# Performance work log

Measured on AMD Instinct MI355X. Metric: run time of the kernel, lower is better.

Reference implementation:

```python
import jax, jax.numpy as jnp
import numpy as np

N = 20000      # nodes
E = 160000     # edges (before self loops)
IN = 128       # in_channels (== edge_dim)
H = 8          # heads
C = 64         # out_channels per head
NEG_SLOPE = 0.2


def setup_inputs() -> dict:
    key = jax.random.key(0)
    ks = jax.random.split(key, 8)
    s_in = np.float32(1.0 / np.sqrt(IN))
    s_att = np.float32(1.0 / np.sqrt(C))
    return {
        "x": jax.random.normal(ks[0], (N, IN), jnp.float32),
        "edge_index": jax.random.randint(ks[1], (2, E), 0, N, dtype=jnp.int32),
        "edge_attr": jax.random.normal(ks[2], (E, IN), jnp.float32),
        "Wl": jax.random.normal(ks[3], (IN, H * C), jnp.float32) * s_in,
        "Wr": jax.random.normal(ks[4], (IN, H * C), jnp.float32) * s_in,
        "We": jax.random.normal(ks[5], (IN, H * C), jnp.float32) * s_in,
        "att": jax.random.normal(ks[6], (H, C), jnp.float32) * s_att,
        "bias": jnp.zeros((H * C,), jnp.float32),
    }


def reference(x, edge_index, edge_attr, Wl, Wr, We, att, bias):
    n = x.shape[0]
    e = edge_attr.shape[0]
    src, dst = edge_index[0], edge_index[1]

    # add self loops; self-loop edge_attr = per-target-node mean of incoming
    # edge attrs (PyG fill_value='mean'); nodes with no in-edges get zeros.
    cnt = jax.ops.segment_sum(jnp.ones((e,), x.dtype), dst, num_segments=n)
    loop_attr = jax.ops.segment_sum(edge_attr, dst, num_segments=n) / jnp.maximum(cnt, 1.0)[:, None]
    loops = jnp.arange(n, dtype=src.dtype)
    src_f = jnp.concatenate([src, loops])          # [E+N]
    dst_f = jnp.concatenate([dst, loops])          # [E+N]
    ea = jnp.concatenate([edge_attr, loop_attr], axis=0)  # [E+N, IN]

    xl = (x @ Wl).reshape(n, H, C)   # source projection
    xr = (x @ Wr).reshape(n, H, C)   # target projection
    xe = (ea @ We).reshape(-1, H, C)  # edge projection

    # GATv2 score: att . LeakyReLU(xl_j + xr_i + xe)
    m = jax.nn.leaky_relu(xl[src_f] + xr[dst_f] + xe, NEG_SLOPE)  # [E+N, H, C]
    logits = jnp.einsum('ehc,hc->eh', m, att)                      # [E+N, H]

    # segment softmax over incoming edges of each target node
    lmax = jax.ops.segment_max(logits, dst_f, num_segments=n)      # [N, H]
    p = jnp.exp(logits - lmax[dst_f])
    denom = jax.ops.segment_sum(p, dst_f, num_segments=n)
    alpha = p / denom[dst_f]                                       # [E+N, H]

    # weighted scatter-add aggregation of source features
    out = jax.ops.segment_sum(alpha[:, :, None] * xl[src_f], dst_f, num_segments=n)
    return out.reshape(n, H * C) + bias
```

## Files before the change

### kernel.cpp

```cpp
#include <hip/hip_runtime.h>

#define N_NODES 20000
#define E_EDGES 160000
#define IN_CH 128
#define H_HEADS 8
#define C_CH 64
#define HC 512
#define M_TOT (E_EDGES + N_NODES)
#define NEG_SLOPE 0.2f
#define NCHUNK ((N_NODES + 255) / 256)

typedef __attribute__((ext_vector_type(8))) short bf16x8;
typedef __attribute__((ext_vector_type(4))) float f32x4;

__device__ __forceinline__ unsigned short f2bf(float f) {
    unsigned u = __float_as_uint(f);
    unsigned r = (u + 0x7FFFu + ((u >> 16) & 1u)) >> 16;
    return (unsigned short)r;
}
__device__ __forceinline__ float bf2f(unsigned short s) {
    return __uint_as_float((unsigned)s << 16);
}
__device__ __forceinline__ float bfx(const bf16x8& v0, const bf16x8& v1, int idx) {
    return bf2f((unsigned short)((idx < 8) ? v0[idx] : v1[idx - 8]));
}

#define GLOAD_LDS16(gsrc, ldst) \
    __builtin_amdgcn_global_load_lds((const __attribute__((address_space(1))) void*)(gsrc), \
                                     (__attribute__((address_space(3))) void*)(ldst), 16, 0, 0)

__global__ void k_deg(const int* __restrict__ ei, int* __restrict__ deg) {
    int e = blockIdx.x * blockDim.x + threadIdx.x;
    if (e >= E_EDGES) return;
    atomicAdd(&deg[ei[E_EDGES + e]], 1);
}

__global__ void k_scan1(const int* __restrict__ deg, int* __restrict__ bsum) {
    __shared__ int red[256];
    int tid = threadIdx.x;
    int i = blockIdx.x * 256 + tid;
    red[tid] = (i < N_NODES) ? deg[i] + 1 : 0;
    __syncthreads();
    for (int off = 128; off > 0; off >>= 1) {
        if (tid < off) red[tid] += red[tid + off];
        __syncthreads();
    }
    if (tid == 0) bsum[blockIdx.x] = red[0];
}

__global__ void k_scan2(const int* __restrict__ bsum, int* __restrict__ boff) {
    if (threadIdx.x == 0) {
        int run = 0;
        for (int b = 0; b < NCHUNK; ++b) { boff[b] = run; run += bsum[b]; }
    }
}

__global__ void k_scan3(const int* __restrict__ deg, const int* __restrict__ boff,
                        int* __restrict__ rowptr, int* __restrict__ cursor,
                        int* __restrict__ eidx, int* __restrict__ src_s,
                        int* __restrict__ dst_s) {
    __shared__ int buf[256];
    int tid = threadIdx.x;
    int i = blockIdx.x * 256 + tid;
    int v = (i < N_NODES) ? deg[i] + 1 : 0;
    buf[tid] = v;
    __syncthreads();
    for (int off = 1; off < 256; off <<= 1) {
        int tv = (tid >= off) ? buf[tid - off] : 0;
        __syncthreads();
        buf[tid] += tv;
        __syncthreads();
    }
    if (i < N_NODES) {
        int excl = boff[blockIdx.x] + buf[tid] - v;
        rowptr[i] = excl;
        eidx[excl] = E_EDGES + i;
        src_s[excl] = i;
        dst_s[excl] = i;
        cursor[i] = excl + 1;
        if (i == N_NODES - 1) rowptr[N_NODES] = excl + v;
    }
}

__global__ void k_fill(const int* __restrict__ ei, int* __restrict__ cursor,
                       int* __restrict__ eidx, int* __restrict__ src_s,
                       int* __restrict__ dst_s) {
    int e = blockIdx.x * blockDim.x + threadIdx.x;
    if (e >= E_EDGES) return;
    int d = ei[E_EDGES + e];
    int slot = atomicAdd(&cursor[d], 1);
    eidx[slot] = e;
    src_s[slot] = ei[e];
    dst_s[slot] = d;
}

__global__ void k_prep(const int* __restrict__ rowptr, const int* __restrict__ eidx,
                       const float* __restrict__ ea, unsigned short* __restrict__ eab) {
    int node = (blockIdx.x * blockDim.x + threadIdx.x) >> 6;
    int lane = threadIdx.x & 63;
    if (node >= N_NODES) return;
    int beg = rowptr[node], end = rowptr[node + 1];
    int cnt = end - beg - 1;
    float s0 = 0.f, s1 = 0.f;
    if (beg + 1 < end) {
        const float* p_nxt = ea + (size_t)eidx[beg + 1] * 128 + lane;
        for (int p = beg + 1; p < end; ++p) {
            const float* cur = p_nxt;
            if (p + 1 < end) p_nxt = ea + (size_t)eidx[p + 1] * 128 + lane;
            float v0 = cur[0], v1 = cur[64];
            s0 += v0; s1 += v1;
            eab[(size_t)p * 128 + lane] = f2bf(v0);
            eab[(size_t)p * 128 + 64 + lane] = f2bf(v1);
        }
    }
    float inv = 1.f / fmaxf((float)cnt, 1.f);
    eab[(size_t)beg * 128 + lane] = f2bf(s0 * inv);
    eab[(size_t)beg * 128 + 64 + lane] = f2bf(s1 * inv);
}

__global__ void k_trans3(const float* __restrict__ Wl, const float* __restrict__ Wr,
                         const float* __restrict__ We,
                         unsigned short* __restrict__ WlT, unsigned short* __restrict__ WrT,
                         unsigned short* __restrict__ WeT) {
    int idx = blockIdx.x * blockDim.x + threadIdx.x;
    if (idx >= HC * IN_CH) return;
    int m = blockIdx.y;
    const float* W = (m == 0) ? Wl : (m == 1) ? Wr : We;
    unsigned short* WT = (m == 0) ? WlT : (m == 1) ? WrT : WeT;
    int n = idx >> 7, k = idx & 127;
    WT[idx] = f2bf(W[(size_t)k * HC + n]);
}

__global__ void k_gemm2(const float* __restrict__ A,
                        const unsigned short* __restrict__ WlT,
                        const unsigned short* __restrict__ WrT,
                        unsigned short* __restrict__ xlb, unsigned short* __restrict__ xrb,
                        int M) {
    __shared__ short As[64 * 128];
    int row0 = blockIdx.x * 64;
    int sel = blockIdx.y >> 1;
    const unsigned short* BT = sel ? WrT : WlT;
    unsigned short* Cb = sel ? xrb : xlb;
    int t = threadIdx.x;
    {
        int row = t >> 2, c0 = (t & 3) * 32;
        int gr = row0 + row;
        int sw = (row & 7) << 4;
        const float* src = A + (size_t)gr * 128 + c0;
        #pragma unroll
        for (int i = 0; i < 4; ++i) {
            bf16x8 v;
            if (gr < M) {
                const float4* p = (const float4*)(src + i * 8);
                float4 f0 = p[0], f1 = p[1];
                v[0] = f2bf(f0.x); v[1] = f2bf(f0.y); v[2] = f2bf(f0.z); v[3] = f2bf(f0.w);
                v[4] = f2bf(f1.x); v[5] = f2bf(f1.y); v[6] = f2bf(f1.z); v[7] = f2bf(f1.w);
            } else {
                #pragma unroll
                for (int j = 0; j < 8; ++j) v[j] = 0;
            }
            int off = row * 256 + (((c0 + i * 8) * 2) ^ sw);
            *(bf16x8*)((char*)As + off) = v;
        }
    }
    __syncthreads();

    int w = t >> 6, l = t & 63;
    int lr = l & 15, lk = l >> 4;
    int col0 = (blockIdx.y & 1) * 256 + w * 64;

    f32x4 acc[4][4];
    #pragma unroll
    for (int mi = 0; mi < 4; ++mi)
        #pragma unroll
        for (int fj = 0; fj < 4; ++fj)
            #pragma unroll
            for (int q = 0; q < 4; ++q) acc[mi][fj][q] = 0.f;

    #pragma unroll
    for (int k0 = 0; k0 < 4; ++k0) {
        bf16x8 a4[4];
        #pragma unroll
        for (int mi = 0; mi < 4; ++mi) {
            int row = mi * 16 + lr;
            int off = row * 256 + ((k0 * 64 + lk * 16) ^ ((row & 7) << 4));
            a4[mi] = *(const bf16x8*)((const char*)As + off);
        }
        #pragma unroll
        for (int fj = 0; fj < 4; ++fj) {
            bf16x8 b = *(const bf16x8*)(BT + (size_t)(col0 + fj * 16 + lr) * 128 + k0 * 32 + lk * 8);
            #pragma unroll
            for (int mi = 0; mi < 4; ++mi)
                acc[mi][fj] = __builtin_amdgcn_mfma_f32_16x16x32_bf16(a4[mi], b, acc[mi][fj], 0, 0, 0);
        }
    }
    #pragma unroll
    for (int mi = 0; mi < 4; ++mi) {
        #pragma unroll
        for (int reg = 0; reg < 4; ++reg) {
            int r = row0 + mi * 16 + lk * 4 + reg;
            if (r < M) {
                unsigned short* cp = Cb + (size_t)r * 512 + col0 + lr;
                #pragma unroll
                for (int fj = 0; fj < 4; ++fj) cp[fj * 16] = f2bf(acc[mi][fj][reg]);
            }
        }
    }
}

#define PREF(R, CB, SLOT) { \
    int s_ = s_src[R], d_ = s_dst[R]; \
    const bf16x8* xp_ = (const bf16x8*)(xlb + (size_t)s_ * 512 + (CB) + q * 16); \
    pa0[SLOT] = xp_[0]; pa1[SLOT] = xp_[1]; \
    const bf16x8* rp_ = (const bf16x8*)(xrb + (size_t)d_ * 512 + (CB) + q * 16); \
    pb0[SLOT] = rp_[0]; pb1[SLOT] = rp_[1]; }

__global__ void k_fused(const int* __restrict__ src_s, const int* __restrict__ dst_s,
                        const int* __restrict__ rowptr,
                        const unsigned short* __restrict__ eab,
                        const unsigned short* __restrict__ WeT,
                        const unsigned short* __restrict__ xlb,
                        const unsigned short* __restrict__ xrb,
                        const float* __restrict__ att, const float* __restrict__ bias,
                        float* __restrict__ logits, float* __restrict__ out) {
    __shared__ short As[64 * 128];
    __shared__ float xeT[4][16][68];
    __shared__ float att_s[512];
    __shared__ float lg[64][8];
    __shared__ int s_src[64], s_dst[64];
    __shared__ int own_node[64], own_beg[64], own_len[64];
    __shared__ int n_own;
    int row0 = blockIdx.x * 64;
    int t = threadIdx.x;

    if (t == 0) n_own = 0;
    __syncthreads();

    {
        int l = t & 63;
        int c_base = (t >> 6) * 4;
        #pragma unroll
        for (int i = 0; i < 4; ++i) {
            int c = c_base + i;
            int row_local = c * 4 + (l >> 4);
            int grow = row0 + row_local;
            if (grow > M_TOT - 1) grow = M_TOT - 1;
            int chunk = (l & 15) ^ (row_local & 7);
            const char* src = (const char*)eab + (size_t)grow * 256 + chunk * 16;
            char* dst = (char*)As + c * 1024;
            GLOAD_LDS16(src, dst);
        }
    }

    if (t < 64) {
        int p = row0 + t;
        int s = 0, d = 0;
        if (p < M_TOT) {
            s = src_s[p]; d = dst_s[p];
            int pb = rowptr[d], pe = rowptr[d + 1];
            if (pb == p && pe <= row0 + 64) {
                int idx = atomicAdd(&n_own, 1);
                own_node[idx] = d; own_beg[idx] = t; own_len[idx] = pe - pb;
            }
        }
        s_src[t] = s; s_dst[t] = d;
    }
    att_s[t] = att[t];
    att_s[t + 256] = att[t + 256];

    asm volatile("s_waitcnt vmcnt(0)");
    __syncthreads();

    int w = t >> 6, l = t & 63;
    int lr = l & 15, lk = l >> 4;
    int eloc = l >> 2, q = l & 3;
    int cb0 = w * 128;

    bf16x8 pa0[2], pa1[2], pb0[2], pb1[2];
    f32x4 acc[4][4];

    PREF(eloc, cb0, 0);

    #pragma unroll
    for (int hh = 0; hh < 2; ++hh) {
        int cb = cb0 + hh * 64;
        int h = w * 2 + hh;

        #pragma unroll
        for (int mi = 0; mi < 4; ++mi)
            #pragma unroll
            for (int fj = 0; fj < 4; ++fj)
                #pragma unroll
                for (int qq = 0; qq < 4; ++qq) acc[mi][fj][qq] = 0.f;

        #pragma unroll
        for (int k0 = 0; k0 < 4; ++k0) {
            bf16x8 a4[4];
            #pragma unroll
            for (int mi = 0; mi < 4; ++mi) {
                int row = mi * 16 + lr;
                int off = row * 256 + ((k0 * 64 + lk * 16) ^ ((row & 7) << 4));
                a4[mi] = *(const bf16x8*)((const char*)As + off);
            }
            #pragma unroll
            for (int fj = 0; fj < 4; ++fj) {
                bf16x8 b = *(const bf16x8*)(WeT + (size_t)(cb + fj * 16 + lr) * 128 + k0 * 32 + lk * 8);
                #pragma unroll
                for (int mi = 0; mi < 4; ++mi)
                    acc[mi][fj] = __builtin_amdgcn_mfma_f32_16x16x32_bf16(a4[mi], b, acc[mi][fj], 0, 0, 0);
            }
        }

        #pragma unroll
        for (int mi = 0; mi < 4; ++mi) {
            if (mi < 3) { PREF(mi * 16 + 16 + eloc, cb, (mi + 1) & 1); }
            else if (hh == 0) { PREF(eloc, cb + 64, 0); }

            #pragma unroll
            for (int fj = 0; fj < 4; ++fj)
                #pragma unroll
                for (int reg = 0; reg < 4; ++reg)
                    xeT[w][lk * 4 + reg][fj * 16 + lr] = acc[mi][fj][reg];

            const bf16x8 ca0 = pa0[mi & 1], ca1 = pa1[mi & 1];
            const bf16x8 cb0v = pb0[mi & 1], cb1v = pb1[mi & 1];

            float sum = 0.f;
            #pragma unroll
            for (int sg = 0; sg < 4; ++sg) {
                float4 xe4 = *(const float4*)&xeT[w][eloc][q * 16 + sg * 4];
                float4 av  = *(const float4*)&att_s[cb + q * 16 + sg * 4];
                float v0 = xe4.x + bfx(ca0, ca1, sg * 4 + 0) + bfx(cb0v, cb1v, sg * 4 + 0);
                float v1 = xe4.y + bfx(ca0, ca1, sg * 4 + 1) + bfx(cb0v, cb1v, sg * 4 + 1);
                float v2 = xe4.z + bfx(ca0, ca1, sg * 4 + 2) + bfx(cb0v, cb1v, sg * 4 + 2);
                float v3 = xe4.w + bfx(ca0, ca1, sg * 4 + 3) + bfx(cb0v, cb1v, sg * 4 + 3);
                v0 = (v0 > 0.f) ? v0 : v0 * NEG_SLOPE;
                v1 = (v1 > 0.f) ? v1 : v1 * NEG_SLOPE;
                v2 = (v2 > 0.f) ? v2 : v2 * NEG_SLOPE;
                v3 = (v3 > 0.f) ? v3 : v3 * NEG_SLOPE;
                sum = fmaf(av.x, v0, sum);
                sum = fmaf(av.y, v1, sum);
                sum = fmaf(av.z, v2, sum);
                sum = fmaf(av.w, v3, sum);
            }
            sum += __shfl_xor(sum, 1, 64);
            sum += __shfl_xor(sum, 2, 64);
            if (q == 0) {
                int rloc = mi * 16 + eloc;
                lg[rloc][h] = sum;
                int p = row0 + rloc;
                if (p < M_TOT) logits[(size_t)p * 8 + h] = sum;
            }
        }
    }
    __syncthreads();

    {
        int lane = t & 63;
        int h = lane >> 3;
        for (int o = w; o < n_own; o += 4) {
            int d = own_node[o], rb = own_beg[o], len = own_len[o];
            float m = -3.4e38f;
            for (int j = 0; j < len; ++j) m = fmaxf(m, lg[rb + j][h]);
            float den = 0.f;
            for (int j = 0; j < len; ++j) den += __expf(lg[rb + j][h] - m);
            float rden = 1.f / den;
            float ac[8] = {};
            bf16x8 v_nxt = *(const bf16x8*)(xlb + (size_t)s_src[rb] * 512 + lane * 8);
            for (int j = 0; j < len; ++j) {
                bf16x8 v = v_nxt;
                if (j + 1 < len)
                    v_nxt = *(const bf16x8*)(xlb + (size_t)s_src[rb + j + 1] * 512 + lane * 8);
                float alpha = __expf(lg[rb + j][h] - m) * rden;
                #pragma unroll
                for (int jj = 0; jj < 8; ++jj) ac[jj] = fmaf(alpha, bf2f((unsigned short)v[jj]), ac[jj]);
            }
            float4* op = (float4*)(out + (size_t)d * 512 + lane * 8);
            const float4* bp = (const float4*)(bias + lane * 8);
            float4 bv0 = bp[0], bv1 = bp[1];
            float4 r0 = { ac[0] + bv0.x, ac[1] + bv0.y, ac[2] + bv0.z, ac[3] + bv0.w };
            float4 r1 = { ac[4] + bv1.x, ac[5] + bv1.y, ac[6] + bv1.z, ac[7] + bv1.w };
            op[0] = r0; op[1] = r1;
        }
    }
}

__global__ void k_cleanup(const int* __restrict__ rowptr, const int* __restrict__ src_s,
                          const float* __restrict__ logits,
                          const unsigned short* __restrict__ xlb, const float* __restrict__ bias,
                          float* __restrict__ out) {
    int node = (blockIdx.x * blockDim.x + threadIdx.x) >> 6;
    int lane = threadIdx.x & 63;
    if (node >= N_NODES) return;
    int beg = rowptr[node], end = rowptr[node + 1];
    if ((beg >> 6) == ((end - 1) >> 6)) return;
    int h = lane >> 3;

    float m = -3.4e38f;
    for (int p = beg; p < end; ++p) m = fmaxf(m, logits[(size_t)p * 8 + h]);
    float den = 0.f;
    for (int p = beg; p < end; ++p) den += __expf(logits[(size_t)p * 8 + h] - m);
    float rden = 1.f / den;

    float acc[8] = {};
    bf16x8 v_nxt = *(const bf16x8*)(xlb + (size_t)src_s[beg] * 512 + lane * 8);
    for (int p = beg; p < end; ++p) {
        bf16x8 v = v_nxt;
        float lgv = logits[(size_t)p * 8 + h];
        if (p + 1 < end)
            v_nxt = *(const bf16x8*)(xlb + (size_t)src_s[p + 1] * 512 + lane * 8);
        float alpha = __expf(lgv - m) * rden;
        #pragma unroll
        for (int j = 0; j < 8; ++j) acc[j] = fmaf(alpha, bf2f((unsigned short)v[j]), acc[j]);
    }
    float4* op = (float4*)(out + (size_t)node * 512 + lane * 8);
    const float4* bp = (const float4*)(bias + lane * 8);
    float4 bv0 = bp[0], bv1 = bp[1];
    float4 r0 = { acc[0] + bv0.x, acc[1] + bv0.y, acc[2] + bv0.z, acc[3] + bv0.w };
    float4 r1 = { acc[4] + bv1.x, acc[5] + bv1.y, acc[6] + bv1.z, acc[7] + bv1.w };
    op[0] = r0; op[1] = r1;
}

extern "C" void kernel_launch(void* const* d_in, const int* in_sizes, int n_in,
                              void* d_out, int out_size, void* d_ws, size_t ws_size,
                              hipStream_t stream) {
    const float* x    = (const float*)d_in[0];
    const int*   ei   = (const int*)d_in[1];
    const float* ea   = (const float*)d_in[2];
    const float* Wl   = (const float*)d_in[3];
    const float* Wr   = (const float*)d_in[4];
    const float* We   = (const float*)d_in[5];
    const float* att  = (const float*)d_in[6];
    const float* bias = (const float*)d_in[7];
    float* out = (float*)d_out;

    unsigned short* xlb = (unsigned short*)d_ws;
    unsigned short* xrb = xlb + (size_t)N_NODES * HC;
    unsigned short* WlT = xrb + (size_t)N_NODES * HC;
    unsigned short* WrT = WlT + HC * IN_CH;
    unsigned short* WeT = WrT + HC * IN_CH;
    unsigned short* eab = WeT + HC * IN_CH;
    float* logits    = (float*)(eab + (size_t)M_TOT * IN_CH);
    int* deg         = (int*)(logits + (size_t)M_TOT * 8);
    int* rowptr      = deg + N_NODES;
    int* cursor      = rowptr + N_NODES + 1;
    int* eidx        = cursor + N_NODES;
    int* src_s       = eidx + M_TOT;
    int* dst_s       = src_s + M_TOT;
    int* bsum        = dst_s + M_TOT;
    int* boff        = bsum + NCHUNK;

    const int B = 256;
    hipMemsetAsync(deg, 0, N_NODES * sizeof(int), stream);
    k_deg<<<(E_EDGES + B - 1) / B, B, 0, stream>>>(ei, deg);
    k_scan1<<<NCHUNK, B, 0, stream>>>(deg, bsum);
    k_scan2<<<1, 64, 0, stream>>>(bsum, boff);
    k_scan3<<<NCHUNK, B, 0, stream>>>(deg, boff, rowptr, cursor, eidx, src_s, dst_s);
    k_fill<<<(E_EDGES + B - 1) / B, B, 0, stream>>>(ei, cursor, eidx, src_s, dst_s);
    k_prep<<<(N_NODES * 64 + B - 1) / B, B, 0, stream>>>(rowptr, eidx, ea, eab);
    k_trans3<<<dim3((HC * IN_CH + B - 1) / B, 3), B, 0, stream>>>(Wl, Wr, We, WlT, WrT, WeT);
    k_gemm2<<<dim3((N_NODES + 63) / 64, 4), B, 0, stream>>>(x, WlT, WrT, xlb, xrb, N_NODES);
    k_fused<<<(M_TOT + 63) / 64, B, 0, stream>>>(src_s, dst_s, rowptr, eab, WeT,
                                                 xlb, xrb, att, bias, logits, out);
    k_cleanup<<<((size_t)N_NODES * 64 + B - 1) / B, B, 0, stream>>>(rowptr, src_s, logits,
                                                                    xlb, bias, out);
}
```

Baseline: 262.8 us.

## Split edge GEMM accumulators in halves, stage xe in bf16, coalesce logits store

The fused edge kernel now computes the edge projection in two halves of 32 rows, so it holds 8 accumulator tiles instead of 16. This is meant to cut register pressure and improve occupancy. The xe staging buffer in shared memory is narrowed from fp32 to truncated bf16, which reduces LDS traffic and footprint but lowers logit precision. Logits are no longer written as scattered per-row global stores; they are written once from the shared lg tile with a coalesced float2 store after the barrier.

Result: no change. 258.7 us (-1.6%).

```diff
diff --git a/kernel.cpp b/kernel.cpp
--- a/kernel.cpp
+++ b/kernel.cpp
@@ -17,6 +17,9 @@
     unsigned u = __float_as_uint(f);
     unsigned r = (u + 0x7FFFu + ((u >> 16) & 1u)) >> 16;
     return (unsigned short)r;
+}
+__device__ __forceinline__ unsigned short f2bf_trunc(float f) {
+    return (unsigned short)(__float_as_uint(f) >> 16);
 }
 __device__ __forceinline__ float bf2f(unsigned short s) {
     return __uint_as_float((unsigned)s << 16);
@@ -224,7 +227,7 @@
                         const float* __restrict__ att, const float* __restrict__ bias,
                         float* __restrict__ logits, float* __restrict__ out) {
     __shared__ short As[64 * 128];
-    __shared__ float xeT[4][16][68];
+    __shared__ unsigned short xeT[4][16][72];
     __shared__ float att_s[512];
     __shared__ float lg[64][8];
     __shared__ int s_src[64], s_dst[64];
@@ -277,7 +280,6 @@
     int cb0 = w * 128;
 
     bf16x8 pa0[2], pa1[2], pb0[2], pb1[2];
-    f32x4 acc[4][4];
 
     PREF(eloc, cb0, 0);
 
@@ -287,73 +289,84 @@
         int h = w * 2 + hh;
 
         #pragma unroll
-        for (int mi = 0; mi < 4; ++mi)
+        for (int mih = 0; mih < 2; ++mih) {
+            f32x4 acc[2][4];
             #pragma unroll
-            for (int fj = 0; fj < 4; ++fj)
-                #pragma unroll
-                for (int qq = 0; qq < 4; ++qq) acc[mi][fj][qq] = 0.f;
-
-        #pragma unroll
-        for (int k0 = 0; k0 < 4; ++k0) {
-            bf16x8 a4[4];
+            for (int mi2 = 0; mi2 < 2; ++mi2)
+                #pragma unroll
+                for (int fj = 0; fj < 4; ++fj)
+                    #pragma unroll
+                    for (int qq = 0; qq < 4; ++qq) acc[mi2][fj][qq] = 0.f;
+
             #pragma unroll
-            for (int mi = 0; mi < 4; ++mi) {
-                int row = mi * 16 + lr;
-                int off = row * 256 + ((k0 * 64 + lk * 16) ^ ((row & 7) << 4));
-                a4[mi] = *(const bf16x8*)((const char*)As + off);
-            }
+            for (int k0 = 0; k0 < 4; ++k0) {
+                bf16x8 a4[2];
+                #pragma unroll
+                for (int mi2 = 0; mi2 < 2; ++mi2) {
+                    int row = (mih * 2 + mi2) * 16 + lr;
+                    int off = row * 256 + ((k0 * 64 + lk * 16) ^ ((row & 7) << 4));
+                    a4[mi2] = *(const bf16x8*)((const char*)As + off);
+                }
+                #pragma unroll
+                for (int fj = 0; fj < 4; ++fj) {
+                    bf16x8 b = *(const bf16x8*)(WeT + (size_t)(cb + fj * 16 + lr) * 128 + k0 * 32 + lk * 8);
+                    #pragma unroll
+                    for (int mi2 = 0; mi2 < 2; ++mi2)
+                        acc[mi2][fj] = __builtin_amdgcn_mfma_f32_16x16x32_bf16(a4[mi2], b, acc[mi2][fj], 0, 0, 0);
+                }
+            }
+
             #pragma unroll
-            for (int fj = 0; fj < 4; ++fj) {
-                bf16x8 b = *(const bf16x8*)(WeT + (size_t)(cb + fj * 16 + lr) * 128 + k0 * 32 + lk * 8);
-                #pragma unroll
-                for (int mi = 0; mi < 4; ++mi)
-                    acc[mi][fj] = __builtin_amdgcn_mfma_f32_16x16x32_bf16(a4[mi], b, acc[mi][fj], 0, 0, 0);
-            }
-        }
-
-        #pragma unroll
-        for (int mi = 0; mi < 4; ++mi) {
-            if (mi < 3) { PREF(mi * 16 + 16 + eloc, cb, (mi + 1) & 1); }
-            else if (hh == 0) { PREF(eloc, cb + 64, 0); }
-
-            #pragma unroll
-            for (int fj = 0; fj < 4; ++fj)
-                #pragma unroll
-                for (int reg = 0; reg < 4; ++reg)
-                    xeT[w][lk * 4 + reg][fj * 16 + lr] = acc[mi][fj][reg];
-
-            const bf16x8 ca0 = pa0[mi & 1], ca1 = pa1[mi & 1];
-            const bf16x8 cb0v = pb0[mi & 1], cb1v = pb1[mi & 1];
-
-            float sum = 0.f;
-            #pragma unroll
-            for (int sg = 0; sg < 4; ++sg) {
-                float4 xe4 = *(const float4*)&xeT[w][eloc][q * 16 + sg * 4];
-                float4 av  = *(const float4*)&att_s[cb + q * 16 + sg * 4];
-                float v0 = xe4.x + bfx(ca0, ca1, sg * 4 + 0) + bfx(cb0v, cb1v, sg * 4 + 0);
-                float v1 = xe4.y + bfx(ca0, ca1, sg * 4 + 1) + bfx(cb0v, cb1v, sg * 4 + 1);
-                float v2 = xe4.z + bfx(ca0, ca1, sg * 4 + 2) + bfx(cb0v, cb1v, sg * 4 + 2);
-                float v3 = xe4.w + bfx(ca0, ca1, sg * 4 + 3) + bfx(cb0v, cb1v, sg * 4 + 3);
-                v0 = (v0 > 0.f) ? v0 : v0 * NEG_SLOPE;
-                v1 = (v1 > 0.f) ? v1 : v1 * NEG_SLOPE;
-                v2 = (v2 > 0.f) ? v2 : v2 * NEG_SLOPE;
-                v3 = (v3 > 0.f) ? v3 : v3 * NEG_SLOPE;
-                sum = fmaf(av.x, v0, sum);
-                sum = fmaf(av.y, v1, sum);
-                sum = fmaf(av.z, v2, sum);
-                sum = fmaf(av.w, v3, sum);
-            }
-            sum += __shfl_xor(sum, 1, 64);
-            sum += __shfl_xor(sum, 2, 64);
-            if (q == 0) {
-                int rloc = mi * 16 + eloc;
-                lg[rloc][h] = sum;
-                int p = row0 + rloc;
-                if (p < M_TOT) logits[(size_t)p * 8 + h] = sum;
-            }
-        }
-    }
-    __syncthreads();
+            for (int mi2 = 0; mi2 < 2; ++mi2) {
+                int mi = mih * 2 + mi2;
+                if (mi < 3) { PREF(mi * 16 + 16 + eloc, cb, (mi + 1) & 1); }
+                else if (hh == 0) { PREF(eloc, cb + 64, 0); }
+
+                #pragma unroll
+                for (int fj = 0; fj < 4; ++fj)
+                    #pragma unroll
+                    for (int reg = 0; reg < 4; ++reg)
+                        xeT[w][lk * 4 + reg][fj * 16 + lr] = f2bf_trunc(acc[mi2][fj][reg]);
+
+                const bf16x8 ca0 = pa0[mi & 1], ca1 = pa1[mi & 1];
+                const bf16x8 cb0v = pb0[mi & 1], cb1v = pb1[mi & 1];
+
+                bf16x8 x0 = *(const bf16x8*)&xeT[w][eloc][q * 16];
+                bf16x8 x1 = *(const bf16x8*)&xeT[w][eloc][q * 16 + 8];
+
+                float sum = 0.f;
+                #pragma unroll
+                for (int sg = 0; sg < 4; ++sg) {
+                    float4 av = *(const float4*)&att_s[cb + q * 16 + sg * 4];
+                    float v0 = bfx(x0, x1, sg * 4 + 0) + bfx(ca0, ca1, sg * 4 + 0) + bfx(cb0v, cb1v, sg * 4 + 0);
+                    float v1 = bfx(x0, x1, sg * 4 + 1) + bfx(ca0, ca1, sg * 4 + 1) + bfx(cb0v, cb1v, sg * 4 + 1);
+                    float v2 = bfx(x0, x1, sg * 4 + 2) + bfx(ca0, ca1, sg * 4 + 2) + bfx(cb0v, cb1v, sg * 4 + 2);
+                    float v3 = bfx(x0, x1, sg * 4 + 3) + bfx(ca0, ca1, sg * 4 + 3) + bfx(cb0v, cb1v, sg * 4 + 3);
+                    v0 = (v0 > 0.f) ? v0 : v0 * NEG_SLOPE;
+                    v1 = (v1 > 0.f) ? v1 : v1 * NEG_SLOPE;
+                    v2 = (v2 > 0.f) ? v2 : v2 * NEG_SLOPE;
+                    v3 = (v3 > 0.f) ? v3 : v3 * NEG_SLOPE;
+                    sum = fmaf(av.x, v0, sum);
+                    sum = fmaf(av.y, v1, sum);
+                    sum = fmaf(av.z, v2, sum);
+                    sum = fmaf(av.w, v3, sum);
+                }
+                sum += __shfl_xor(sum, 1, 64);
+                sum += __shfl_xor(sum, 2, 64);
+                if (q == 0) lg[mi * 16 + eloc][h] = sum;
+            }
+        }
+    }
+    __syncthreads();
+
+    {
+        int nval = (M_TOT - row0 < 64 ? M_TOT - row0 : 64) * 8;
+        if (t * 2 < nval) {
+            const float* lf = (const float*)lg;
+            float2 v = { lf[t * 2], lf[t * 2 + 1] };
+            *(float2*)(logits + (size_t)row0 * 8 + t * 2) = v;
+        }
+    }
 
     {
         int lane = t & 63;
@@ -457,7 +470,7 @@
     k_scan2<<<1, 64, 0, stream>>>(bsum, boff);
     k_scan3<<<NCHUNK, B, 0, stream>>>(deg, boff, rowptr, cursor, eidx, src_s, dst_s);
     k_fill<<<(E_EDGES + B - 1) / B, B, 0, stream>>>(ei, cursor, eidx, src_s, dst_s);
-    k_prep<<<(N_NODES * 64 + B - 1) / B, B, 0, stream>>>(rowptr, eidx, ea, eab);
+    k_prep<<<((size_t)N_NODES * 64 + B - 1) / B, B, 0, stream>>>(rowptr, eidx, ea, eab);
     k_trans3<<<dim3((HC * IN_CH + B - 1) / B, 3), B, 0, stream>>>(Wl, Wr, We, WlT, WrT, WeT);
     k_gemm2<<<dim3((N_NODES + 63) / 64, 4), B, 0, stream>>>(x, WlT, WrT, xlb, xrb, N_NODES);
     k_fused<<<(M_TOT + 63) / 64, B, 0, stream>>>(src_s, dst_s, rowptr, eab, WeT,
```

## Split fused attention kernel across head halves and pack edge metadata into int4

Applied to the files above, without the earlier changes.

The fused edge kernel now runs on a 2D grid, with each block handling 4 of the 8 heads instead of looping over 2 heads per wave. This doubles the number of blocks and lowers per-block register and LDS pressure, at the cost of loading the edge-attribute tile twice. Logits are stored in a per-half [2][M][4] layout. The LDS xe staging buffer is switched to truncated bf16, which loses some precision. The separate eidx/src/dst arrays are merged into one int4 array so each edge's metadata comes from a single vector load.

Result: faster. 247.7 us (-5.8%).

```diff
diff --git a/kernel.cpp b/kernel.cpp
--- a/kernel.cpp
+++ b/kernel.cpp
@@ -11,12 +11,16 @@
 #define NCHUNK ((N_NODES + 255) / 256)
 
 typedef __attribute__((ext_vector_type(8))) short bf16x8;
+typedef __attribute__((ext_vector_type(4))) short bf16x4;
 typedef __attribute__((ext_vector_type(4))) float f32x4;
 
 __device__ __forceinline__ unsigned short f2bf(float f) {
     unsigned u = __float_as_uint(f);
     unsigned r = (u + 0x7FFFu + ((u >> 16) & 1u)) >> 16;
     return (unsigned short)r;
+}
+__device__ __forceinline__ unsigned short f2bf_trunc(float f) {
+    return (unsigned short)(__float_as_uint(f) >> 16);
 }
 __device__ __forceinline__ float bf2f(unsigned short s) {
     return __uint_as_float((unsigned)s << 16);
@@ -57,8 +61,7 @@
 
 __global__ void k_scan3(const int* __restrict__ deg, const int* __restrict__ boff,
                         int* __restrict__ rowptr, int* __restrict__ cursor,
-                        int* __restrict__ eidx, int* __restrict__ src_s,
-                        int* __restrict__ dst_s) {
+                        int4* __restrict__ edat) {
     __shared__ int buf[256];
     int tid = threadIdx.x;
     int i = blockIdx.x * 256 + tid;
@@ -74,27 +77,22 @@
     if (i < N_NODES) {
         int excl = boff[blockIdx.x] + buf[tid] - v;
         rowptr[i] = excl;
-        eidx[excl] = E_EDGES + i;
-        src_s[excl] = i;
-        dst_s[excl] = i;
+        edat[excl] = make_int4(E_EDGES + i, i, i, 0);
         cursor[i] = excl + 1;
         if (i == N_NODES - 1) rowptr[N_NODES] = excl + v;
     }
 }
 
 __global__ void k_fill(const int* __restrict__ ei, int* __restrict__ cursor,
-                       int* __restrict__ eidx, int* __restrict__ src_s,
-                       int* __restrict__ dst_s) {
+                       int4* __restrict__ edat) {
     int e = blockIdx.x * blockDim.x + threadIdx.x;
     if (e >= E_EDGES) return;
     int d = ei[E_EDGES + e];
     int slot = atomicAdd(&cursor[d], 1);
-    eidx[slot] = e;
-    src_s[slot] = ei[e];
-    dst_s[slot] = d;
-}
-
-__global__ void k_prep(const int* __restrict__ rowptr, const int* __restrict__ eidx,
+    edat[slot] = make_int4(e, ei[e], d, 0);
+}
+
+__global__ void k_prep(const int* __restrict__ rowptr, const int4* __restrict__ edat,
                        const float* __restrict__ ea, unsigned short* __restrict__ eab) {
     int node = (blockIdx.x * blockDim.x + threadIdx.x) >> 6;
     int lane = threadIdx.x & 63;
@@ -103,10 +101,10 @@
     int cnt = end - beg - 1;
     float s0 = 0.f, s1 = 0.f;
     if (beg + 1 < end) {
-        const float* p_nxt = ea + (size_t)eidx[beg + 1] * 128 + lane;
+        const float* p_nxt = ea + (size_t)edat[beg + 1].x * 128 + lane;
         for (int p = beg + 1; p < end; ++p) {
             const float* cur = p_nxt;
-            if (p + 1 < end) p_nxt = ea + (size_t)eidx[p + 1] * 128 + lane;
+            if (p + 1 < end) p_nxt = ea + (size_t)edat[p + 1].x * 128 + lane;
             float v0 = cur[0], v1 = cur[64];
             s0 += v0; s1 += v1;
             eab[(size_t)p * 128 + lane] = f2bf(v0);
@@ -215,22 +213,22 @@
     const bf16x8* rp_ = (const bf16x8*)(xrb + (size_t)d_ * 512 + (CB) + q * 16); \
     pb0[SLOT] = rp_[0]; pb1[SLOT] = rp_[1]; }
 
-__global__ void k_fused(const int* __restrict__ src_s, const int* __restrict__ dst_s,
-                        const int* __restrict__ rowptr,
+__global__ void k_fused(const int4* __restrict__ edat, const int* __restrict__ rowptr,
                         const unsigned short* __restrict__ eab,
                         const unsigned short* __restrict__ WeT,
                         const unsigned short* __restrict__ xlb,
                         const unsigned short* __restrict__ xrb,
                         const float* __restrict__ att, const float* __restrict__ bias,
-                        float* __restrict__ logits, float* __restrict__ out) {
+                        float* __restrict__ lq, float* __restrict__ out) {
     __shared__ short As[64 * 128];
-    __shared__ float xeT[4][16][68];
-    __shared__ float att_s[512];
-    __shared__ float lg[64][8];
+    __shared__ unsigned short xeT[4][16][72];
+    __shared__ float att_s[256];
+    __shared__ float lg[64][4];
     __shared__ int s_src[64], s_dst[64];
     __shared__ int own_node[64], own_beg[64], own_len[64];
     __shared__ int n_own;
     int row0 = blockIdx.x * 64;
+    int y = blockIdx.y;
     int t = threadIdx.x;
 
     if (t == 0) n_own = 0;
@@ -256,7 +254,8 @@
         int p = row0 + t;
         int s = 0, d = 0;
         if (p < M_TOT) {
-            s = src_s[p]; d = dst_s[p];
+            int4 v = edat[p];
+            s = v.y; d = v.z;
             int pb = rowptr[d], pe = rowptr[d + 1];
             if (pb == p && pe <= row0 + 64) {
                 int idx = atomicAdd(&n_own, 1);
@@ -265,8 +264,7 @@
         }
         s_src[t] = s; s_dst[t] = d;
     }
-    att_s[t] = att[t];
-    att_s[t + 256] = att[t + 256];
+    att_s[t & 255] = att[y * 256 + (t & 255)];
 
     asm volatile("s_waitcnt vmcnt(0)");
     __syncthreads();
@@ -274,119 +272,117 @@
     int w = t >> 6, l = t & 63;
     int lr = l & 15, lk = l >> 4;
     int eloc = l >> 2, q = l & 3;
-    int cb0 = w * 128;
+    int h = y * 4 + w;
+    int cb = h * 64;
 
     bf16x8 pa0[2], pa1[2], pb0[2], pb1[2];
     f32x4 acc[4][4];
 
-    PREF(eloc, cb0, 0);
-
-    #pragma unroll
-    for (int hh = 0; hh < 2; ++hh) {
-        int cb = cb0 + hh * 64;
-        int h = w * 2 + hh;
-
-        #pragma unroll
-        for (int mi = 0; mi < 4; ++mi)
+    PREF(eloc, cb, 0);
+
+    #pragma unroll
+    for (int mi = 0; mi < 4; ++mi)
+        #pragma unroll
+        for (int fj = 0; fj < 4; ++fj)
             #pragma unroll
-            for (int fj = 0; fj < 4; ++fj)
-                #pragma unroll
-                for (int qq = 0; qq < 4; ++qq) acc[mi][fj][qq] = 0.f;
-
-        #pragma unroll
-        for (int k0 = 0; k0 < 4; ++k0) {
-            bf16x8 a4[4];
+            for (int qq = 0; qq < 4; ++qq) acc[mi][fj][qq] = 0.f;
+
+    #pragma unroll
+    for (int k0 = 0; k0 < 4; ++k0) {
+        bf16x8 a4[4];
+        #pragma unroll
+        for (int mi = 0; mi < 4; ++mi) {
+            int row = mi * 16 + lr;
+            int off = row * 256 + ((k0 * 64 + lk * 16) ^ ((row & 7) << 4));
+            a4[mi] = *(const bf16x8*)((const char*)As + off);
+        }
+        #pragma unroll
+        for (int fj = 0; fj < 4; ++fj) {
+            bf16x8 b = *(const bf16x8*)(WeT + (size_t)(cb + fj * 16 + lr) * 128 + k0 * 32 + lk * 8);
             #pragma unroll
-            for (int mi = 0; mi < 4; ++mi) {
-                int row = mi * 16 + lr;
-                int off = row * 256 + ((k0 * 64 + lk * 16) ^ ((row & 7) << 4));
-                a4[mi] = *(const bf16x8*)((const char*)As + off);
-            }
+            for (int mi = 0; mi < 4; ++mi)
+                acc[mi][fj] = __builtin_amdgcn_mfma_f32_16x16x32_bf16(a4[mi], b, acc[mi][fj], 0, 0, 0);
+        }
+    }
+
+    #pragma unroll
+    for (int mi = 0; mi < 4; ++mi) {
+        if (mi < 3) { PREF(mi * 16 + 16 + eloc, cb, (mi + 1) & 1); }
+
+        #pragma unroll
+        for (int fj = 0; fj < 4; ++fj)
             #pragma unroll
-            for (int fj = 0; fj < 4; ++fj) {
-                bf16x8 b = *(const bf16x8*)(WeT + (size_t)(cb + fj * 16 + lr) * 128 + k0 * 32 + lk * 8);
-                #pragma unroll
-                for (int mi = 0; mi < 4; ++mi)
-                    acc[mi][fj] = __builtin_amdgcn_mfma_f32_16x16x32_bf16(a4[mi], b, acc[mi][fj], 0, 0, 0);
-            }
-        }
-
-        #pragma unroll
-        for (int mi = 0; mi < 4; ++mi) {
-            if (mi < 3) { PREF(mi * 16 + 16 + eloc, cb, (mi + 1) & 1); }
-            else if (hh == 0) { PREF(eloc, cb + 64, 0); }
-
-            #pragma unroll
-            for (int fj = 0; fj < 4; ++fj)
-                #pragma unroll
-                for (int reg = 0; reg < 4; ++reg)
-                    xeT[w][lk * 4 + reg][fj * 16 + lr] = acc[mi][fj][reg];
-
-            const bf16x8 ca0 = pa0[mi & 1], ca1 = pa1[mi & 1];
-            const bf16x8 cb0v = pb0[mi & 1], cb1v = pb1[mi & 1];
-
-            float sum = 0.f;
-            #pragma unroll
-            for (int sg = 0; sg < 4; ++sg) {
-                float4 xe4 = *(const float4*)&xeT[w][eloc][q * 16 + sg * 4];
-                float4 av  = *(const float4*)&att_s[cb + q * 16 + sg * 4];
-                float v0 = xe4.x + bfx(ca0, ca1, sg * 4 + 0) + bfx(cb0v, cb1v, sg * 4 + 0);
-                float v1 = xe4.y + bfx(ca0, ca1, sg * 4 + 1) + bfx(cb0v, cb1v, sg * 4 + 1);
-                float v2 = xe4.z + bfx(ca0, ca1, sg * 4 + 2) + bfx(cb0v, cb1v, sg * 4 + 2);
-                float v3 = xe4.w + bfx(ca0, ca1, sg * 4 + 3) + bfx(cb0v, cb1v, sg * 4 + 3);
-                v0 = (v0 > 0.f) ? v0 : v0 * NEG_SLOPE;
-                v1 = (v1 > 0.f) ? v1 : v1 * NEG_SLOPE;
-                v2 = (v2 > 0.f) ? v2 : v2 * NEG_SLOPE;
-                v3 = (v3 > 0.f) ? v3 : v3 * NEG_SLOPE;
-                sum = fmaf(av.x, v0, sum);
-                sum = fmaf(av.y, v1, sum);
-                sum = fmaf(av.z, v2, sum);
-                sum = fmaf(av.w, v3, sum);
-            }
-            sum += __shfl_xor(sum, 1, 64);
-            sum += __shfl_xor(sum, 2, 64);
-            if (q == 0) {
-                int rloc = mi * 16 + eloc;
-                lg[rloc][h] = sum;
-                int p = row0 + rloc;
-                if (p < M_TOT) logits[(size_t)p * 8 + h] = sum;
-            }
-        }
-    }
-    __syncthreads();
+            for (int reg = 0; reg < 4; ++reg)
+                xeT[w][lk * 4 + reg][fj * 16 + lr] = f2bf_trunc(acc[mi][fj][reg]);
+
+        const bf16x8 ca0 = pa0[mi & 1], ca1 = pa1[mi & 1];
+        const bf16x8 cb0v = pb0[mi & 1], cb1v = pb1[mi & 1];
+
+        bf16x8 x0 = *(const bf16x8*)&xeT[w][eloc][q * 16];
+        bf16x8 x1 = *(const bf16x8*)&xeT[w][eloc][q * 16 + 8];
+
+        float sum = 0.f;
+        #pragma unroll
+        for (int sg = 0; sg < 4; ++sg) {
+            float4 av = *(const float4*)&att_s[w * 64 + q * 16 + sg * 4];
+            float v0 = bfx(x0, x1, sg * 4 + 0) + bfx(ca0, ca1, sg * 4 + 0) + bfx(cb0v, cb1v, sg * 4 + 0);
+            float v1 = bfx(x0, x1, sg * 4 + 1) + bfx(ca0, ca1, sg * 4 + 1) + bfx(cb0v, cb1v, sg * 4 + 1);
+            float v2 = bfx(x0, x1, sg * 4 + 2) + bfx(ca0, ca1, sg * 4 + 2) + bfx(cb0v, cb1v, sg * 4 + 2);
+            float v3 = bfx(x0, x1, sg * 4 + 3) + bfx(ca0, ca1, sg * 4 + 3) + bfx(cb0v, cb1v, sg * 4 + 3);
+            v0 = (v0 > 0.f) ? v0 : v0 * NEG_SLOPE;
+            v1 = (v1 > 0.f) ? v1 : v1 * NEG_SLOPE;
+            v2 = (v2 > 0.f) ? v2 : v2 * NEG_SLOPE;
+            v3 = (v3 > 0.f) ? v3 : v3 * NEG_SLOPE;
+            sum = fmaf(av.x, v0, sum);
+            sum = fmaf(av.y, v1, sum);
+            sum = fmaf(av.z, v2, sum);
+            sum = fmaf(av.w, v3, sum);
+        }
+        sum += __shfl_xor(sum, 1, 64);
+        sum += __shfl_xor(sum, 2, 64);
+        if (q == 0) lg[mi * 16 + eloc][w] = sum;
+    }
+    __syncthreads();
+
+    if (t < 64) {
+        int p = row0 + t;
+        if (p < M_TOT) {
+            const float4* lr4 = (const float4*)&lg[t][0];
+            *(float4*)(lq + ((size_t)y * M_TOT + p) * 4) = lr4[0];
+        }
+    }
 
     {
         int lane = t & 63;
-        int h = lane >> 3;
+        int hl = lane >> 4;
+        int coff = y * 256 + lane * 4;
         for (int o = w; o < n_own; o += 4) {
             int d = own_node[o], rb = own_beg[o], len = own_len[o];
             float m = -3.4e38f;
-            for (int j = 0; j < len; ++j) m = fmaxf(m, lg[rb + j][h]);
+            for (int j = 0; j < len; ++j) m = fmaxf(m, lg[rb + j][hl]);
             float den = 0.f;
-            for (int j = 0; j < len; ++j) den += __expf(lg[rb + j][h] - m);
+            for (int j = 0; j < len; ++j) den += __expf(lg[rb + j][hl] - m);
             float rden = 1.f / den;
-            float ac[8] = {};
-            bf16x8 v_nxt = *(const bf16x8*)(xlb + (size_t)s_src[rb] * 512 + lane * 8);
+            float ac[4] = {};
+            bf16x4 v_nxt = *(const bf16x4*)(xlb + (size_t)s_src[rb] * 512 + coff);
             for (int j = 0; j < len; ++j) {
-                bf16x8 v = v_nxt;
+                bf16x4 v = v_nxt;
                 if (j + 1 < len)
-                    v_nxt = *(const bf16x8*)(xlb + (size_t)s_src[rb + j + 1] * 512 + lane * 8);
-                float alpha = __expf(lg[rb + j][h] - m) * rden;
+                    v_nxt = *(const bf16x4*)(xlb + (size_t)s_src[rb + j + 1] * 512 + coff);
+                float alpha = __expf(lg[rb + j][hl] - m) * rden;
                 #pragma unroll
-                for (int jj = 0; jj < 8; ++jj) ac[jj] = fmaf(alpha, bf2f((unsigned short)v[jj]), ac[jj]);
+                for (int jj = 0; jj < 4; ++jj) ac[jj] = fmaf(alpha, bf2f((unsigned short)v[jj]), ac[jj]);
             }
-            float4* op = (float4*)(out + (size_t)d * 512 + lane * 8);
-            const float4* bp = (const float4*)(bias + lane * 8);
-            float4 bv0 = bp[0], bv1 = bp[1];
-            float4 r0 = { ac[0] + bv0.x, ac[1] + bv0.y, ac[2] + bv0.z, ac[3] + bv0.w };
-            float4 r1 = { ac[4] + bv1.x, ac[5] + bv1.y, ac[6] + bv1.z, ac[7] + bv1.w };
-            op[0] = r0; op[1] = r1;
-        }
-    }
-}
-
-__global__ void k_cleanup(const int* __restrict__ rowptr, const int* __restrict__ src_s,
-                          const float* __restrict__ logits,
+            const float4* bp = (const float4*)(bias + coff);
+            float4 bv = bp[0];
+            float4 r0 = { ac[0] + bv.x, ac[1] + bv.y, ac[2] + bv.z, ac[3] + bv.w };
+            *(float4*)(out + (size_t)d * 512 + coff) = r0;
+        }
+    }
+}
+
+__global__ void k_cleanup(const int* __restrict__ rowptr, const int4* __restrict__ edat,
+                          const float* __restrict__ lq,
                           const unsigned short* __restrict__ xlb, const float* __restrict__ bias,
                           float* __restrict__ out) {
     int node = (blockIdx.x * blockDim.x + threadIdx.x) >> 6;
@@ -395,20 +391,21 @@
     int beg = rowptr[node], end = rowptr[node + 1];
     if ((beg >> 6) == ((end - 1) >> 6)) return;
     int h = lane >> 3;
+    const float* lp = lq + (size_t)(h >> 2) * M_TOT * 4 + (h & 3);
 
     float m = -3.4e38f;
-    for (int p = beg; p < end; ++p) m = fmaxf(m, logits[(size_t)p * 8 + h]);
+    for (int p = beg; p < end; ++p) m = fmaxf(m, lp[(size_t)p * 4]);
     float den = 0.f;
-    for (int p = beg; p < end; ++p) den += __expf(logits[(size_t)p * 8 + h] - m);
+    for (int p = beg; p < end; ++p) den += __expf(lp[(size_t)p * 4] - m);
     float rden = 1.f / den;
 
     float acc[8] = {};
-    bf16x8 v_nxt = *(const bf16x8*)(xlb + (size_t)src_s[beg] * 512 + lane * 8);
+    bf16x8 v_nxt = *(const bf16x8*)(xlb + (size_t)edat[beg].y * 512 + lane * 8);
     for (int p = beg; p < end; ++p) {
         bf16x8 v = v_nxt;
-        float lgv = logits[(size_t)p * 8 + h];
+        float lgv = lp[(size_t)p * 4];
         if (p + 1 < end)
-            v_nxt = *(const bf16x8*)(xlb + (size_t)src_s[p + 1] * 512 + lane * 8);
+            v_nxt = *(const bf16x8*)(xlb + (size_t)edat[p + 1].y * 512 + lane * 8);
         float alpha = __expf(lgv - m) * rden;
         #pragma unroll
         for (int j = 0; j < 8; ++j) acc[j] = fmaf(alpha, bf2f((unsigned short)v[j]), acc[j]);
@@ -440,14 +437,12 @@
     unsigned short* WrT = WlT + HC * IN_CH;
     unsigned short* WeT = WrT + HC * IN_CH;
     unsigned short* eab = WeT + HC * IN_CH;
-    float* logits    = (float*)(eab + (size_t)M_TOT * IN_CH);
-    int* deg         = (int*)(logits + (size_t)M_TOT * 8);
+    float* lq        = (float*)(eab + (size_t)M_TOT * IN_CH);
+    int4* edat       = (int4*)(lq + (size_t)2 * M_TOT * 4);
+    int* deg         = (int*)(edat + M_TOT);
     int* rowptr      = deg + N_NODES;
     int* cursor      = rowptr + N_NODES + 1;
-    int* eidx        = cursor + N_NODES;
-    int* src_s       = eidx + M_TOT;
-    int* dst_s       = src_s + M_TOT;
-    int* bsum        = dst_s + M_TOT;
+    int* bsum        = cursor + N_NODES;
     int* boff        = bsum + NCHUNK;
 
     const int B = 256;
@@ -455,13 +450,13 @@
     k_deg<<<(E_EDGES + B - 1) / B, B, 0, stream>>>(ei, deg);
     k_scan1<<<NCHUNK, B, 0, stream>>>(deg, bsum);
     k_scan2<<<1, 64, 0, stream>>>(bsum, boff);
-    k_scan3<<<NCHUNK, B, 0, stream>>>(deg, boff, rowptr, cursor, eidx, src_s, dst_s);
-    k_fill<<<(E_EDGES + B - 1) / B, B, 0, stream>>>(ei, cursor, eidx, src_s, dst_s);
-    k_prep<<<(N_NODES * 64 + B - 1) / B, B, 0, stream>>>(rowptr, eidx, ea, eab);
+    k_scan3<<<NCHUNK, B, 0, stream>>>(deg, boff, rowptr, cursor, edat);
+    k_fill<<<(E_EDGES + B - 1) / B, B, 0, stream>>>(ei, cursor, edat);
+    k_prep<<<((size_t)N_NODES * 64 + B - 1) / B, B, 0, stream>>>(rowptr, edat, ea, eab);
     k_trans3<<<dim3((HC * IN_CH + B - 1) / B, 3), B, 0, stream>>>(Wl, Wr, We, WlT, WrT, WeT);
     k_gemm2<<<dim3((N_NODES + 63) / 64, 4), B, 0, stream>>>(x, WlT, WrT, xlb, xrb, N_NODES);
-    k_fused<<<(M_TOT + 63) / 64, B, 0, stream>>>(src_s, dst_s, rowptr, eab, WeT,
-                                                 xlb, xrb, att, bias, logits, out);
-    k_cleanup<<<((size_t)N_NODES * 64 + B - 1) / B, B, 0, stream>>>(rowptr, src_s, logits,
+    k_fused<<<dim3((M_TOT + 63) / 64, 2), B, 0, stream>>>(edat, rowptr, eab, WeT,
+                                                          xlb, xrb, att, bias, lq, out);
+    k_cleanup<<<((size_t)N_NODES * 64 + B - 1) / B, B, 0, stream>>>(rowptr, edat, lq,
                                                                     xlb, bias, out);
 }
```
